# Kernel tuning notes

Measured on AMD Instinct MI355X. Metric: run time of the kernel, lower is better.

## Reference

```python
import jax, jax.numpy as jnp
import numpy as np

B, S, HID = 2, 2048, 2048
H, KV, D = 8, 2, 256
SW = 512                      # sliding window
SCALAR = 256.0                # query_pre_attn_scalar
EPS = 1e-6
THETA = 1000000.0             # global rope theta
SOFTCAP = 30.0


def _layernorm_unit(x, eps=EPS):
    # Gemma3nRMSNorm with_scale=False == LayerNorm with unit weight, no bias (fp32)
    x = x.astype(jnp.float32)
    mu = jnp.mean(x, axis=-1, keepdims=True)
    xc = x - mu
    var = jnp.mean(xc * xc, axis=-1, keepdims=True)
    return xc * jax.lax.rsqrt(var + eps)


def _rope_cache(seq_len, head_dim, theta):
    inv_freq = 1.0 / (theta ** (jnp.arange(0, head_dim, 2, dtype=jnp.float32) / head_dim))
    pos = jnp.arange(seq_len, dtype=jnp.float32)
    freqs = pos[:, None] * inv_freq[None, :]          # [S, D/2]
    emb = jnp.concatenate([freqs, freqs], axis=-1)    # [S, D]
    return jnp.cos(emb), jnp.sin(emb)


def _rotate_half(x):
    x1, x2 = jnp.split(x, 2, axis=-1)
    return jnp.concatenate([-x2, x1], axis=-1)


def setup_inputs() -> dict:
    key = jax.random.key(0)
    ks = jax.random.split(key, 5)
    sc = 0.02
    return {
        "hidden_states": jax.random.normal(ks[0], (B, S, HID), dtype=jnp.float32),
        "Wq": jax.random.normal(ks[1], (H * D, HID), dtype=jnp.float32) * sc,
        "Wk": jax.random.normal(ks[2], (KV * D, HID), dtype=jnp.float32) * sc,
        "Wv": jax.random.normal(ks[3], (KV * D, HID), dtype=jnp.float32) * sc,
        "Wo": jax.random.normal(ks[4], (HID, HID), dtype=jnp.float32) * sc,
    }


def reference(hidden_states, Wq, Wk, Wv, Wo):
    b, s, _ = hidden_states.shape
    # projections (nn.Linear: y = x @ W.T)
    q = jnp.einsum('bsh,oh->bso', hidden_states, Wq).reshape(b, s, H, D).transpose(0, 2, 1, 3)
    k = jnp.einsum('bsh,oh->bso', hidden_states, Wk).reshape(b, s, KV, D).transpose(0, 2, 1, 3)
    v = jnp.einsum('bsh,oh->bso', hidden_states, Wv).reshape(b, s, KV, D).transpose(0, 2, 1, 3)

    # rotary (applied BEFORE qk norm, as in the source)
    cos, sin = _rope_cache(s, D, THETA)  # [S, D]
    cos = cos[None, None]                # [1,1,S,D]
    sin = sin[None, None]
    q = q * cos + _rotate_half(q) * sin
    k = k * cos + _rotate_half(k) * sin

    # per-head norms, then query scaling
    q = _layernorm_unit(q) * SCALAR
    k = _layernorm_unit(k)
    v = _layernorm_unit(v)

    # GQA: expand kv heads
    rep = H // KV
    k = jnp.repeat(k, rep, axis=1)
    v = jnp.repeat(v, rep, axis=1)

    scores = jnp.einsum('bhqd,bhkd->bhqk', q, k) / jnp.sqrt(jnp.float32(D))

    # sliding-window causal mask: allow j in (i - SW, i]
    i = jnp.arange(s)[:, None]
    j = jnp.arange(s)[None, :]
    allowed = (j <= i) & (j > i - SW)
    mask = jnp.where(allowed, 0.0, -jnp.inf).astype(scores.dtype)
    scores = scores + mask

    # soft-capping: tanh(-inf/30)*30 = -30, so masked positions get -30 (matches torch)
    scores = jnp.tanh(scores / SOFTCAP) * SOFTCAP
    probs = jax.nn.softmax(scores.astype(jnp.float32), axis=-1).astype(v.dtype)

    out = jnp.einsum('bhqk,bhkd->bhqd', probs, v)
    out = out.transpose(0, 2, 1, 3).reshape(b, s, H * D)
    return jnp.einsum('bso,ho->bsh', out, Wo)
```

## Files before the change

kernel.cpp:

```cpp
#include <hip/hip_runtime.h>
#include <hip/hip_bf16.h>
#include <math.h>

#define BB 2
#define SS 2048
#define HIDD 2048
#define NH 8
#define NKVH 2
#define HD 256
#define SWIN 512
#define QSCALAR 256.0f
#define LEPS 1e-6f
#define SCAP 30.0f
#define EXPM60 8.75651076269652e-27f

typedef short bfx8 __attribute__((ext_vector_type(8)));
typedef float f32x4 __attribute__((ext_vector_type(4)));
typedef ushort u16x8 __attribute__((ext_vector_type(8)));

__device__ __forceinline__ ushort f2bf(float f) {
    uint u = __float_as_uint(f);
    return (ushort)((u + 0x7fffu + ((u >> 16) & 1u)) >> 16);
}
__device__ __forceinline__ float bf2f(ushort h) {
    return __uint_as_float(((uint)h) << 16);
}

__global__ __launch_bounds__(256) void cvt_hi(
    const float* __restrict__ x, ushort* __restrict__ hi, int n4)
{
    int i = (int)blockIdx.x * 256 + (int)threadIdx.x;
    if (i >= n4) return;
    float4 v = ((const float4*)x)[i];
    ushort4 h;
    h.x = f2bf(v.x); h.y = f2bf(v.y); h.z = f2bf(v.z); h.w = f2bf(v.w);
    ((ushort4*)hi)[i] = h;
}

__device__ __forceinline__ void stage_tile(
    const ushort* __restrict__ g, int ldg, int grow0, int k0,
    ushort* lds, int w, int lane)
{
    #pragma unroll
    for (int j = 0; j < 2; ++j) {
        const int rr = w * 32 + j * 16;
        const ushort* src = g + (size_t)(grow0 + rr + (lane >> 2)) * ldg
                              + k0 + ((lane & 3) << 3);
        __builtin_amdgcn_global_load_lds(
            (const __attribute__((address_space(1))) void*)src,
            (__attribute__((address_space(3))) void*)((char*)lds + rr * 64),
            16, 0, 0);
    }
}

__global__ __launch_bounds__(256) void gemm_bf16(
    const ushort* __restrict__ Ah, const ushort* __restrict__ Bh,
    float* __restrict__ C0, float* __restrict__ C1, float* __restrict__ C2,
    int n0, int n1, int n2, int K)
{
    __shared__ __align__(16) ushort Ah_s[128 * 32];
    __shared__ __align__(16) ushort Bh_s[128 * 32];

    const int tid  = (int)threadIdx.x;
    const int w    = tid >> 6;
    const int lane = tid & 63;
    const int wr = w >> 1, wc = w & 1;
    const int lm = lane & 15, lk = lane >> 4;

    const int row0  = (int)blockIdx.x * 128;
    const int gcol0 = (int)blockIdx.y * 128;

    int col0 = gcol0;
    float* C; int ldc;
    if (col0 < n0)           { C = C0; ldc = n0; }
    else if (col0 < n0 + n1) { C = C1; ldc = n1; col0 -= n0; }
    else                     { C = C2; ldc = n2; col0 -= (n0 + n1); }

    f32x4 acc[4][4];
    #pragma unroll
    for (int m = 0; m < 4; ++m)
        #pragma unroll
        for (int n = 0; n < 4; ++n) acc[m][n] = (f32x4)0.f;

    for (int k0 = 0; k0 < K; k0 += 32) {
        stage_tile(Ah, K, row0, k0, Ah_s, w, lane);
        stage_tile(Bh, K, gcol0, k0, Bh_s, w, lane);
        __syncthreads();

        bfx8 ah[4], bh[4];
        #pragma unroll
        for (int m = 0; m < 4; ++m) {
            ah[m] = *(const bfx8*)&Ah_s[(wr * 64 + m * 16 + lm) * 32 + lk * 8];
            bh[m] = *(const bfx8*)&Bh_s[(wc * 64 + m * 16 + lm) * 32 + lk * 8];
        }
        #pragma unroll
        for (int m = 0; m < 4; ++m)
            #pragma unroll
            for (int n = 0; n < 4; ++n)
                acc[m][n] = __builtin_amdgcn_mfma_f32_16x16x32_bf16(
                    ah[m], bh[n], acc[m][n], 0, 0, 0);
        __syncthreads();
    }

    #pragma unroll
    for (int m = 0; m < 4; ++m) {
        const int row = row0 + wr * 64 + m * 16 + lk * 4;
        #pragma unroll
        for (int n = 0; n < 4; ++n) {
            float* cp = C + (size_t)row * ldc + col0 + wc * 64 + n * 16 + lm;
            #pragma unroll
            for (int r = 0; r < 4; ++r) cp[(size_t)r * ldc] = acc[m][n][r];
        }
    }
}

__global__ __launch_bounds__(256) void rope_norm(
    const float* __restrict__ qb, const float* __restrict__ kb, float* __restrict__ vb,
    ushort* __restrict__ Qo, ushort* __restrict__ Ko)
{
    const int row  = (int)blockIdx.x * 4 + ((int)threadIdx.x >> 6);
    const int lane = (int)threadIdx.x & 63;
    const int t  = row / 12;
    const int hh = row - t * 12;
    const int pos = t & (SS - 1);

    const float* src;
    size_t oidx;
    int mode;
    if (hh < 8)       { oidx = ((size_t)t << 11) + (hh << 8) + (lane << 2);        src = qb + oidx; mode = 0; }
    else if (hh < 10) { oidx = ((size_t)t << 9) + ((hh - 8) << 8) + (lane << 2);   src = kb + oidx; mode = 1; }
    else              { oidx = ((size_t)t << 9) + ((hh - 10) << 8) + (lane << 2);  src = vb + oidx; mode = 2; }

    float x[4];
    *(float4*)x = *(const float4*)src;

    if (mode < 2) {
        float oth[4];
        #pragma unroll
        for (int e = 0; e < 4; ++e) oth[e] = __shfl_xor(x[e], 32);
        #pragma unroll
        for (int e = 0; e < 4; ++e) {
            const int d = (lane << 2) + e;
            const int f = d & 127;
            const float invf = (float)exp2(-(double)f * (19.931568569324174 / 128.0));
            const float ang = (float)pos * invf;
            float sv, cv;
            sincosf(ang, &sv, &cv);
            const float rot = (lane < 32) ? -oth[e] : oth[e];
            x[e] = fmaf(x[e], cv, rot * sv);
        }
    }

    float s1 = x[0] + x[1] + x[2] + x[3];
    #pragma unroll
    for (int off = 1; off < 64; off <<= 1) s1 += __shfl_xor(s1, off);
    const float mu = s1 * (1.0f / 256.0f);
    float y[4];
    float s2 = 0.f;
    #pragma unroll
    for (int e = 0; e < 4; ++e) { y[e] = x[e] - mu; s2 = fmaf(y[e], y[e], s2); }
    #pragma unroll
    for (int off = 1; off < 64; off <<= 1) s2 += __shfl_xor(s2, off);
    const float rstd = rsqrtf(s2 * (1.0f / 256.0f) + LEPS);
    const float sc = (mode == 0) ? rstd * QSCALAR : rstd;
    #pragma unroll
    for (int e = 0; e < 4; ++e) y[e] *= sc;

    if (mode == 2) {
        *(float4*)(vb + oidx) = *(float4*)y;
    } else {
        ushort4 h4;
        h4.x = f2bf(y[0]); h4.y = f2bf(y[1]); h4.z = f2bf(y[2]); h4.w = f2bf(y[3]);
        if (mode == 0) *(ushort4*)(Qo + oidx) = h4;
        else           *(ushort4*)(Ko + oidx) = h4;
    }
}

__global__ __launch_bounds__(256) void vtrans(
    const float* __restrict__ vb, ushort* __restrict__ Vt)
{
    __shared__ float T[256][33];
    const int bk = (int)blockIdx.x & 3, st = (int)blockIdx.x >> 2;
    const int b = bk >> 1, kv = bk & 1;
    const int tid = (int)threadIdx.x;

    #pragma unroll
    for (int i = 0; i < 8; ++i) {
        int idx = tid + i * 256;
        int s = idx >> 6, c4 = idx & 63;
        float4 v = *(const float4*)(vb + ((size_t)(b * 2048 + st * 32 + s)) * 512 + kv * 256 + c4 * 4);
        T[c4 * 4 + 0][s] = v.x; T[c4 * 4 + 1][s] = v.y;
        T[c4 * 4 + 2][s] = v.z; T[c4 * 4 + 3][s] = v.w;
    }
    __syncthreads();

    const int d = tid;
    ushort h[32];
    #pragma unroll
    for (int s = 0; s < 32; ++s) h[s] = f2bf(T[d][s]);
    size_t off = ((size_t)bk * 256 + d) * 2048 + st * 32;
    #pragma unroll
    for (int j = 0; j < 4; ++j)
        *(u16x8*)(Vt + off + j * 8) = *(u16x8*)&h[j * 8];
}

__global__ __launch_bounds__(256) void vcum_part(
    const float* __restrict__ vb, float* __restrict__ Vpart)
{
    const int bk = (int)blockIdx.x >> 6, ch = (int)blockIdx.x & 63;
    const int b = bk >> 1, kv = bk & 1, d = (int)threadIdx.x;
    const float* p = vb + ((size_t)(b * 2048 + ch * 32)) * 512 + kv * 256 + d;
    float s = 0.f;
    #pragma unroll 8
    for (int j = 0; j < 32; ++j) s += p[(size_t)j * 512];
    Vpart[((size_t)(bk * 64 + ch)) * 256 + d] = s;
}

__global__ __launch_bounds__(256) void vcum_scan(
    const float* __restrict__ Vpart, float* __restrict__ Vcum)
{
    const int bk = (int)blockIdx.x, d = (int)threadIdx.x;
    float run = 0.f;
    Vcum[((size_t)(bk * 65)) * 256 + d] = 0.f;
    for (int c2 = 0; c2 < 64; ++c2) {
        run += Vpart[((size_t)(bk * 64 + c2)) * 256 + d];
        Vcum[((size_t)(bk * 65 + c2 + 1)) * 256 + d] = run;
    }
}

__device__ __forceinline__ void attn_stage(
    const ushort* __restrict__ Kb, const ushort* __restrict__ Vt,
    ushort* Ks, ushort* Vs, int b, int kv, int bk, int kc, int w, int lane)
{
    #pragma unroll
    for (int ii = 0; ii < 4; ++ii) {
        const int islot = w * 4 + ii;
        {
            const int key = islot * 2 + (lane >> 5);
            const int g = (lane & 31) ^ (key & 7);
            const size_t src = ((size_t)(b * 2048 + kc + key)) * 512 + kv * 256 + g * 8;
            __builtin_amdgcn_global_load_lds(
                (const __attribute__((address_space(1))) void*)(Kb + src),
                (__attribute__((address_space(3))) void*)((char*)Ks + islot * 1024), 16, 0, 0);
        }
        {
            const int d = islot * 16 + (lane >> 2);
            const int g = (lane & 3) ^ (d & 3);
            const size_t src = ((size_t)(bk * 256 + d)) * 2048 + kc + g * 8;
            __builtin_amdgcn_global_load_lds(
                (const __attribute__((address_space(1))) void*)(Vt + src),
                (__attribute__((address_space(3))) void*)((char*)Vs + islot * 1024), 16, 0, 0);
        }
    }
}

__global__ __launch_bounds__(256, 2) void attn_mfma(
    const ushort* __restrict__ Qb, const ushort* __restrict__ Kb,
    const ushort* __restrict__ Vt, const float* __restrict__ Vcum,
    ushort* __restrict__ ao)
{
    __shared__ __align__(16) ushort K_s[2][32 * 256];
    __shared__ __align__(16) ushort V_s[2][256 * 32];
    __shared__ __align__(16) ushort P_s[4][16 * 32];

    const int tid = (int)threadIdx.x;
    const int w = tid >> 6, lane = tid & 63;
    const int c = lane & 15, lk = lane >> 4;
    const int bh = (int)blockIdx.y, b = bh >> 3, h = bh & 7, kv = h >> 2;
    const int bk = b * 2 + kv;
    const int q0 = (int)blockIdx.x * 64;

    const int ks0  = (q0 >= SWIN) ? (q0 - SWIN) : 0;
    const int kend = q0 + 64;
    const int nch  = (kend - ks0) >> 5;

    bfx8 qf[8];
    {
        const size_t qoff = ((size_t)(b * SS + q0 + w * 16 + c)) * 2048 + h * 256 + lk * 8;
        #pragma unroll
        for (int ks = 0; ks < 8; ++ks) qf[ks] = *(const bfx8*)(Qb + qoff + ks * 32);
    }

    f32x4 acc_o[16];
    #pragma unroll
    for (int i = 0; i < 16; ++i) acc_o[i] = (f32x4)0.f;
    float l_r[4] = {0.f, 0.f, 0.f, 0.f};

    attn_stage(Kb, Vt, K_s[0], V_s[0], b, kv, bk, ks0, w, lane);
    __syncthreads();

    int cur = 0;
    for (int t = 0; t < nch; ++t) {
        const int kc = ks0 + t * 32;
        if (t + 1 < nch)
            attn_stage(Kb, Vt, K_s[cur ^ 1], V_s[cur ^ 1], b, kv, bk, kc + 32, w, lane);

        f32x4 acc_s[2] = {(f32x4)0.f, (f32x4)0.f};
        #pragma unroll
        for (int ks = 0; ks < 8; ++ks) {
            #pragma unroll
            for (int n = 0; n < 2; ++n) {
                const int key = n * 16 + c;
                const int gi = (ks * 4 + lk) ^ (key & 7);
                const bfx8 kf = *(const bfx8*)&K_s[cur][key * 256 + gi * 8];
                acc_s[n] = __builtin_amdgcn_mfma_f32_16x16x32_bf16(qf[ks], kf, acc_s[n], 0, 0, 0);
            }
        }

        #pragma unroll
        for (int r = 0; r < 4; ++r) {
            const int irow = q0 + w * 16 + lk * 4 + r;
            #pragma unroll
            for (int n = 0; n < 2; ++n) {
                const int j = kc + n * 16 + c;
                const float sp = acc_s[n][r] * (1.f / 16.f);
                const float t1 = __expf(sp * (2.f / SCAP));
                const float pe = __expf(-2.f * SCAP / (t1 + 1.f));
                const bool ok = (j <= irow) && (j > irow - SWIN);
                const float pp = ok ? pe : EXPM60;
                l_r[r] += pp;
                const int row = lk * 4 + r;
                const int gi = (2 * n + (c >> 3)) ^ (row & 3) ^ (row >> 2);
                P_s[w][row * 32 + gi * 8 + (c & 7)] = f2bf(pp);
            }
        }
        asm volatile("s_waitcnt lgkmcnt(0)" ::: "memory");
        __builtin_amdgcn_sched_barrier(0);

        {
            const int gia = lk ^ (c & 3) ^ (c >> 2);
            const bfx8 pa = *(const bfx8*)&P_s[w][c * 32 + gia * 8];
            #pragma unroll
            for (int nn = 0; nn < 16; ++nn) {
                const int d = nn * 16 + c;
                const int gv = lk ^ (d & 3);
                const bfx8 vf = *(const bfx8*)&V_s[cur][d * 32 + gv * 8];
                acc_o[nn] = __builtin_amdgcn_mfma_f32_16x16x32_bf16(pa, vf, acc_o[nn], 0, 0, 0);
            }
        }
        __syncthreads();
        cur ^= 1;
    }

    #pragma unroll
    for (int r = 0; r < 4; ++r) {
        float s = l_r[r];
        s += __shfl_xor(s, 1); s += __shfl_xor(s, 2);
        s += __shfl_xor(s, 4); s += __shfl_xor(s, 8);
        l_r[r] = s;
    }
    const int cs = ks0 >> 5, ce = kend >> 5;
    const float nout = (float)(SS - (kend - ks0));
    float inv[4];
    #pragma unroll
    for (int r = 0; r < 4; ++r) inv[r] = 1.f / (l_r[r] + nout * EXPM60);

    #pragma unroll
    for (int nn = 0; nn < 16; ++nn) {
        const int d = nn * 16 + c;
        const size_t vco = ((size_t)bk * 65) * 256 + d;
        const float U = (Vcum[vco + (size_t)64 * 256] - Vcum[vco + (size_t)ce * 256])
                      + Vcum[vco + (size_t)cs * 256];
        #pragma unroll
        for (int r = 0; r < 4; ++r) {
            const int row = q0 + w * 16 + lk * 4 + r;
            const float ov = (acc_o[nn][r] + EXPM60 * U) * inv[r];
            ao[((size_t)(b * SS + row)) * 2048 + h * 256 + d] = f2bf(ov);
        }
    }
}

extern "C" void kernel_launch(void* const* d_in, const int* in_sizes, int n_in,
                              void* d_out, int out_size, void* d_ws, size_t ws_size,
                              hipStream_t stream)
{
    (void)in_sizes; (void)n_in; (void)out_size; (void)ws_size;
    const float* hs = (const float*)d_in[0];
    const float* Wq = (const float*)d_in[1];
    const float* Wk = (const float*)d_in[2];
    const float* Wv = (const float*)d_in[3];
    const float* Wo = (const float*)d_in[4];
    float* out = (float*)d_out;

    const size_t MiB = 1024 * 1024;
    char* p = (char*)d_ws;
    ushort* hsb = (ushort*)(p);
    ushort* wkb = (ushort*)(p + 16 * MiB);
    ushort* wob = (ushort*)(p + 28 * MiB);
    float*  qb  = (float*)(p + 36 * MiB);
    float*  kb  = (float*)(p + 68 * MiB);
    float*  vb  = (float*)(p + 76 * MiB);
    ushort* Qo  = (ushort*)(p + 84 * MiB);
    ushort* Ko  = (ushort*)(p + 100 * MiB);
    ushort* ao    = hsb;
    ushort* Vt    = wkb;
    float*  Vcum  = (float*)(p + 20 * MiB);
    float*  Vpart = (float*)(p + 21 * MiB);

    cvt_hi<<<8192, 256, 0, stream>>>(hs, hsb, 2097152);
    cvt_hi<<<4096, 256, 0, stream>>>(Wq, wkb, 1048576);
    cvt_hi<<<1024, 256, 0, stream>>>(Wk, wkb + 4194304, 262144);
    cvt_hi<<<1024, 256, 0, stream>>>(Wv, wkb + 5242880, 262144);
    cvt_hi<<<4096, 256, 0, stream>>>(Wo, wob, 1048576);

    gemm_bf16<<<dim3(32, 24), 256, 0, stream>>>(
        hsb, wkb, qb, kb, vb, 2048, 512, 512, 2048);

    rope_norm<<<12288, 256, 0, stream>>>(qb, kb, vb, Qo, Ko);

    vtrans   <<<256, 256, 0, stream>>>(vb, Vt);
    vcum_part<<<256, 256, 0, stream>>>(vb, Vpart);
    vcum_scan<<<4, 256, 0, stream>>>(Vpart, Vcum);

    attn_mfma<<<dim3(32, 16), 256, 0, stream>>>(Qo, Ko, Vt, Vcum, ao);

    gemm_bf16<<<dim3(32, 16), 256, 0, stream>>>(
        ao, wob, out, out, out, 2048, 0, 0, 2048);
}
```

Baseline: 333.8 us.

## Merge conversion kernels, fuse V prefix sums, double attention query tile

The five fp32-to-bf16 conversion launches become one kernel, and the per-chunk V column sums move into the transpose kernel so vcum_part is no longer launched. Rope now uses fast float exp2f and __sincosf in place of a double exp2 and precise sincosf. The attention kernel gives each wave 32 query rows (128 per block), so every staged K/V tile feeds twice as many MFMAs and fewer KV chunks are loaded per query. In exchange the block holds twice the accumulators with launch bounds lowered to one block per SIMD, only 256 attention blocks are launched, and the fast sincos loses accuracy at large angles.

After: 330.2 us. Within noise of the previous version (-1.1%).

```diff
diff --git a/kernel.cpp b/kernel.cpp
--- a/kernel.cpp
+++ b/kernel.cpp
@@ -26,15 +26,23 @@
     return __uint_as_float(((uint)h) << 16);
 }
 
-__global__ __launch_bounds__(256) void cvt_hi(
-    const float* __restrict__ x, ushort* __restrict__ hi, int n4)
-{
-    int i = (int)blockIdx.x * 256 + (int)threadIdx.x;
-    if (i >= n4) return;
-    float4 v = ((const float4*)x)[i];
+__global__ __launch_bounds__(256) void cvt_all(
+    const float* __restrict__ hs, const float* __restrict__ Wq,
+    const float* __restrict__ Wk, const float* __restrict__ Wv,
+    const float* __restrict__ Wo,
+    ushort* __restrict__ hsb, ushort* __restrict__ wkb, ushort* __restrict__ wob)
+{
+    const int i = (int)blockIdx.x * 256 + (int)threadIdx.x;
+    const float* s; ushort* d; int off;
+    if (i < 2097152)      { s = hs; d = hsb;           off = i; }
+    else if (i < 3145728) { s = Wq; d = wkb;           off = i - 2097152; }
+    else if (i < 3407872) { s = Wk; d = wkb + 4194304; off = i - 3145728; }
+    else if (i < 3670016) { s = Wv; d = wkb + 5242880; off = i - 3407872; }
+    else                  { s = Wo; d = wob;           off = i - 3670016; }
+    float4 v = ((const float4*)s)[off];
     ushort4 h;
     h.x = f2bf(v.x); h.y = f2bf(v.y); h.z = f2bf(v.z); h.w = f2bf(v.w);
-    ((ushort4*)hi)[i] = h;
+    ((ushort4*)d)[off] = h;
 }
 
 __device__ __forceinline__ void stage_tile(
@@ -142,10 +150,10 @@
         for (int e = 0; e < 4; ++e) {
             const int d = (lane << 2) + e;
             const int f = d & 127;
-            const float invf = (float)exp2(-(double)f * (19.931568569324174 / 128.0));
+            const float invf = exp2f(-(float)f * (19.931568569324174f / 128.0f));
             const float ang = (float)pos * invf;
             float sv, cv;
-            sincosf(ang, &sv, &cv);
+            __sincosf(ang, &sv, &cv);
             const float rot = (lane < 32) ? -oth[e] : oth[e];
             x[e] = fmaf(x[e], cv, rot * sv);
         }
@@ -177,7 +185,7 @@
 }
 
 __global__ __launch_bounds__(256) void vtrans(
-    const float* __restrict__ vb, ushort* __restrict__ Vt)
+    const float* __restrict__ vb, ushort* __restrict__ Vt, float* __restrict__ Vpart)
 {
     __shared__ float T[256][33];
     const int bk = (int)blockIdx.x & 3, st = (int)blockIdx.x >> 2;
@@ -196,24 +204,18 @@
 
     const int d = tid;
     ushort h[32];
-    #pragma unroll
-    for (int s = 0; s < 32; ++s) h[s] = f2bf(T[d][s]);
+    float psum = 0.f;
+    #pragma unroll
+    for (int s = 0; s < 32; ++s) {
+        const float x = T[d][s];
+        h[s] = f2bf(x);
+        psum += x;
+    }
     size_t off = ((size_t)bk * 256 + d) * 2048 + st * 32;
     #pragma unroll
     for (int j = 0; j < 4; ++j)
         *(u16x8*)(Vt + off + j * 8) = *(u16x8*)&h[j * 8];
-}
-
-__global__ __launch_bounds__(256) void vcum_part(
-    const float* __restrict__ vb, float* __restrict__ Vpart)
-{
-    const int bk = (int)blockIdx.x >> 6, ch = (int)blockIdx.x & 63;
-    const int b = bk >> 1, kv = bk & 1, d = (int)threadIdx.x;
-    const float* p = vb + ((size_t)(b * 2048 + ch * 32)) * 512 + kv * 256 + d;
-    float s = 0.f;
-    #pragma unroll 8
-    for (int j = 0; j < 32; ++j) s += p[(size_t)j * 512];
-    Vpart[((size_t)(bk * 64 + ch)) * 256 + d] = s;
+    Vpart[((size_t)(bk * 64 + st)) * 256 + d] = psum;
 }
 
 __global__ __launch_bounds__(256) void vcum_scan(
@@ -254,37 +256,41 @@
     }
 }
 
-__global__ __launch_bounds__(256, 2) void attn_mfma(
+__global__ __launch_bounds__(256, 1) void attn_mfma(
     const ushort* __restrict__ Qb, const ushort* __restrict__ Kb,
     const ushort* __restrict__ Vt, const float* __restrict__ Vcum,
     ushort* __restrict__ ao)
 {
     __shared__ __align__(16) ushort K_s[2][32 * 256];
     __shared__ __align__(16) ushort V_s[2][256 * 32];
-    __shared__ __align__(16) ushort P_s[4][16 * 32];
+    __shared__ __align__(16) ushort P_s[4][2][16 * 32];
 
     const int tid = (int)threadIdx.x;
     const int w = tid >> 6, lane = tid & 63;
     const int c = lane & 15, lk = lane >> 4;
     const int bh = (int)blockIdx.y, b = bh >> 3, h = bh & 7, kv = h >> 2;
     const int bk = b * 2 + kv;
-    const int q0 = (int)blockIdx.x * 64;
+    const int q0 = (int)blockIdx.x * 128;
+    const int wq0 = q0 + w * 32;
 
     const int ks0  = (q0 >= SWIN) ? (q0 - SWIN) : 0;
-    const int kend = q0 + 64;
+    const int kend = q0 + 128;
     const int nch  = (kend - ks0) >> 5;
 
-    bfx8 qf[8];
-    {
-        const size_t qoff = ((size_t)(b * SS + q0 + w * 16 + c)) * 2048 + h * 256 + lk * 8;
-        #pragma unroll
-        for (int ks = 0; ks < 8; ++ks) qf[ks] = *(const bfx8*)(Qb + qoff + ks * 32);
-    }
-
-    f32x4 acc_o[16];
-    #pragma unroll
-    for (int i = 0; i < 16; ++i) acc_o[i] = (f32x4)0.f;
-    float l_r[4] = {0.f, 0.f, 0.f, 0.f};
+    bfx8 qf[2][8];
+    #pragma unroll
+    for (int rg = 0; rg < 2; ++rg) {
+        const size_t qoff = ((size_t)(b * SS + wq0 + rg * 16 + c)) * 2048 + h * 256 + lk * 8;
+        #pragma unroll
+        for (int ks = 0; ks < 8; ++ks) qf[rg][ks] = *(const bfx8*)(Qb + qoff + ks * 32);
+    }
+
+    f32x4 acc_o[2][16];
+    #pragma unroll
+    for (int rg = 0; rg < 2; ++rg)
+        #pragma unroll
+        for (int i = 0; i < 16; ++i) acc_o[rg][i] = (f32x4)0.f;
+    float l_r[2][4] = {{0.f, 0.f, 0.f, 0.f}, {0.f, 0.f, 0.f, 0.f}};
 
     attn_stage(Kb, Vt, K_s[0], V_s[0], b, kv, bk, ks0, w, lane);
     __syncthreads();
@@ -295,7 +301,7 @@
         if (t + 1 < nch)
             attn_stage(Kb, Vt, K_s[cur ^ 1], V_s[cur ^ 1], b, kv, bk, kc + 32, w, lane);
 
-        f32x4 acc_s[2] = {(f32x4)0.f, (f32x4)0.f};
+        f32x4 acc_s[2][2] = {{(f32x4)0.f, (f32x4)0.f}, {(f32x4)0.f, (f32x4)0.f}};
         #pragma unroll
         for (int ks = 0; ks < 8; ++ks) {
             #pragma unroll
@@ -303,39 +309,44 @@
                 const int key = n * 16 + c;
                 const int gi = (ks * 4 + lk) ^ (key & 7);
                 const bfx8 kf = *(const bfx8*)&K_s[cur][key * 256 + gi * 8];
-                acc_s[n] = __builtin_amdgcn_mfma_f32_16x16x32_bf16(qf[ks], kf, acc_s[n], 0, 0, 0);
+                acc_s[0][n] = __builtin_amdgcn_mfma_f32_16x16x32_bf16(qf[0][ks], kf, acc_s[0][n], 0, 0, 0);
+                acc_s[1][n] = __builtin_amdgcn_mfma_f32_16x16x32_bf16(qf[1][ks], kf, acc_s[1][n], 0, 0, 0);
             }
         }
 
         #pragma unroll
-        for (int r = 0; r < 4; ++r) {
-            const int irow = q0 + w * 16 + lk * 4 + r;
-            #pragma unroll
-            for (int n = 0; n < 2; ++n) {
-                const int j = kc + n * 16 + c;
-                const float sp = acc_s[n][r] * (1.f / 16.f);
-                const float t1 = __expf(sp * (2.f / SCAP));
-                const float pe = __expf(-2.f * SCAP / (t1 + 1.f));
-                const bool ok = (j <= irow) && (j > irow - SWIN);
-                const float pp = ok ? pe : EXPM60;
-                l_r[r] += pp;
-                const int row = lk * 4 + r;
-                const int gi = (2 * n + (c >> 3)) ^ (row & 3) ^ (row >> 2);
-                P_s[w][row * 32 + gi * 8 + (c & 7)] = f2bf(pp);
+        for (int rg = 0; rg < 2; ++rg)
+            #pragma unroll
+            for (int r = 0; r < 4; ++r) {
+                const int irow = wq0 + rg * 16 + lk * 4 + r;
+                #pragma unroll
+                for (int n = 0; n < 2; ++n) {
+                    const int j = kc + n * 16 + c;
+                    const float sp = acc_s[rg][n][r] * (1.f / 16.f);
+                    const float t1 = __expf(sp * (2.f / SCAP));
+                    const float pe = __expf(-2.f * SCAP / (t1 + 1.f));
+                    const bool ok = (j <= irow) && (j > irow - SWIN);
+                    const float pp = ok ? pe : EXPM60;
+                    l_r[rg][r] += pp;
+                    const int row = lk * 4 + r;
+                    const int gi = (2 * n + (c >> 3)) ^ (row & 3) ^ (row >> 2);
+                    P_s[w][rg][row * 32 + gi * 8 + (c & 7)] = f2bf(pp);
+                }
             }
-        }
         asm volatile("s_waitcnt lgkmcnt(0)" ::: "memory");
         __builtin_amdgcn_sched_barrier(0);
 
         {
             const int gia = lk ^ (c & 3) ^ (c >> 2);
-            const bfx8 pa = *(const bfx8*)&P_s[w][c * 32 + gia * 8];
+            const bfx8 pa0 = *(const bfx8*)&P_s[w][0][c * 32 + gia * 8];
+            const bfx8 pa1 = *(const bfx8*)&P_s[w][1][c * 32 + gia * 8];
             #pragma unroll
             for (int nn = 0; nn < 16; ++nn) {
                 const int d = nn * 16 + c;
                 const int gv = lk ^ (d & 3);
                 const bfx8 vf = *(const bfx8*)&V_s[cur][d * 32 + gv * 8];
-                acc_o[nn] = __builtin_amdgcn_mfma_f32_16x16x32_bf16(pa, vf, acc_o[nn], 0, 0, 0);
+                acc_o[0][nn] = __builtin_amdgcn_mfma_f32_16x16x32_bf16(pa0, vf, acc_o[0][nn], 0, 0, 0);
+                acc_o[1][nn] = __builtin_amdgcn_mfma_f32_16x16x32_bf16(pa1, vf, acc_o[1][nn], 0, 0, 0);
             }
         }
         __syncthreads();
@@ -343,17 +354,22 @@
     }
 
     #pragma unroll
-    for (int r = 0; r < 4; ++r) {
-        float s = l_r[r];
-        s += __shfl_xor(s, 1); s += __shfl_xor(s, 2);
-        s += __shfl_xor(s, 4); s += __shfl_xor(s, 8);
-        l_r[r] = s;
-    }
+    for (int rg = 0; rg < 2; ++rg)
+        #pragma unroll
+        for (int r = 0; r < 4; ++r) {
+            float s = l_r[rg][r];
+            s += __shfl_xor(s, 1); s += __shfl_xor(s, 2);
+            s += __shfl_xor(s, 4); s += __shfl_xor(s, 8);
+            l_r[rg][r] = s;
+        }
     const int cs = ks0 >> 5, ce = kend >> 5;
     const float nout = (float)(SS - (kend - ks0));
-    float inv[4];
-    #pragma unroll
-    for (int r = 0; r < 4; ++r) inv[r] = 1.f / (l_r[r] + nout * EXPM60);
+    float inv[2][4];
+    #pragma unroll
+    for (int rg = 0; rg < 2; ++rg)
+        #pragma unroll
+        for (int r = 0; r < 4; ++r)
+            inv[rg][r] = 1.f / (l_r[rg][r] + nout * EXPM60);
 
     #pragma unroll
     for (int nn = 0; nn < 16; ++nn) {
@@ -362,11 +378,13 @@
         const float U = (Vcum[vco + (size_t)64 * 256] - Vcum[vco + (size_t)ce * 256])
                       + Vcum[vco + (size_t)cs * 256];
         #pragma unroll
-        for (int r = 0; r < 4; ++r) {
-            const int row = q0 + w * 16 + lk * 4 + r;
-            const float ov = (acc_o[nn][r] + EXPM60 * U) * inv[r];
-            ao[((size_t)(b * SS + row)) * 2048 + h * 256 + d] = f2bf(ov);
-        }
+        for (int rg = 0; rg < 2; ++rg)
+            #pragma unroll
+            for (int r = 0; r < 4; ++r) {
+                const int row = wq0 + rg * 16 + lk * 4 + r;
+                const float ov = (acc_o[rg][nn][r] + EXPM60 * U) * inv[rg][r];
+                ao[((size_t)(b * SS + row)) * 2048 + h * 256 + d] = f2bf(ov);
+            }
     }
 }
 
@@ -397,22 +415,17 @@
     float*  Vcum  = (float*)(p + 20 * MiB);
     float*  Vpart = (float*)(p + 21 * MiB);
 
-    cvt_hi<<<8192, 256, 0, stream>>>(hs, hsb, 2097152);
-    cvt_hi<<<4096, 256, 0, stream>>>(Wq, wkb, 1048576);
-    cvt_hi<<<1024, 256, 0, stream>>>(Wk, wkb + 4194304, 262144);
-    cvt_hi<<<1024, 256, 0, stream>>>(Wv, wkb + 5242880, 262144);
-    cvt_hi<<<4096, 256, 0, stream>>>(Wo, wob, 1048576);
+    cvt_all<<<18432, 256, 0, stream>>>(hs, Wq, Wk, Wv, Wo, hsb, wkb, wob);
 
     gemm_bf16<<<dim3(32, 24), 256, 0, stream>>>(
         hsb, wkb, qb, kb, vb, 2048, 512, 512, 2048);
 
     rope_norm<<<12288, 256, 0, stream>>>(qb, kb, vb, Qo, Ko);
 
-    vtrans   <<<256, 256, 0, stream>>>(vb, Vt);
-    vcum_part<<<256, 256, 0, stream>>>(vb, Vpart);
+    vtrans   <<<256, 256, 0, stream>>>(vb, Vt, Vpart);
     vcum_scan<<<4, 256, 0, stream>>>(Vpart, Vcum);
 
-    attn_mfma<<<dim3(32, 16), 256, 0, stream>>>(Qo, Ko, Vt, Vcum, ao);
+    attn_mfma<<<dim3(16, 16), 256, 0, stream>>>(Qo, Ko, Vt, Vcum, ao);
 
     gemm_bf16<<<dim3(32, 16), 256, 0, stream>>>(
         ao, wob, out, out, out, 2048, 0, 0, 2048);
```
